# Optimization experiments

Measured on AMD Instinct MI355X. Metric: run time of the kernel, lower is better.

## Reference

```python
import jax, jax.numpy as jnp
import numpy as np

EPS = 1e-12  # tf.nn.l2_normalize epsilon used by keras Dot(normalize=True)

def _l2_normalize(x):
    # x: [..., D]; matches tf.nn.l2_normalize: x * rsqrt(max(sum(x^2), eps))
    sq = jnp.sum(x * x, axis=-1, keepdims=True)
    return x * jax.lax.rsqrt(jnp.maximum(sq, EPS))

def setup_inputs() -> dict:
    key = jax.random.key(0)
    k1, k2, k3 = jax.random.split(key, 3)
    B, L, D = 16, 1024, 1024
    a = jax.random.normal(k1, (B, L, D), dtype=jnp.float32)
    b = jax.random.normal(k2, (B, L, D), dtype=jnp.float32)
    # keras 'uniform' initializer: U(-0.05, 0.05)
    kernel = jax.random.uniform(k3, (D, 1), dtype=jnp.float32, minval=-0.05, maxval=0.05)
    return {"a": a, "b": b, "kernel": kernel}

def reference(a, b, kernel):
    # kernel: [D, 1] -> broadcastable weight vector [D]
    w = kernel[:, 0]
    # elementwise kernel weighting of both sequences: [B, L, D]
    ra = _l2_normalize(a * w)
    rb = _l2_normalize(b * w)
    # cosine-similarity matrix over sequence positions: [B, L, L]
    return jnp.einsum('bid,bjd->bij', ra, rb)
```

## Files before the change

### kernel.cpp

```cpp
#include <hip/hip_runtime.h>
#include <hip/hip_bf16.h>


typedef __bf16 bf16x8 __attribute__((ext_vector_type(8)));
typedef float f32x4 __attribute__((ext_vector_type(4)));

__device__ __forceinline__ unsigned short f2bf(float f) {
  __hip_bfloat16 h = __float2bfloat16(f);
  return *reinterpret_cast<unsigned short*>(&h);
}

__device__ __forceinline__ void gload16(const void* g, void* ldsp) {
  __builtin_amdgcn_global_load_lds(
      (const __attribute__((address_space(1))) unsigned int*)g,
      (__attribute__((address_space(3))) unsigned int*)ldsp,
      16, 0, 0);
}

__global__ void __launch_bounds__(256)
norm_scale_kernel(const float* __restrict__ a, const float* __restrict__ b,
                  const float* __restrict__ w, unsigned short* __restrict__ ra,
                  unsigned short* __restrict__ rb) {
  const int wave = threadIdx.x >> 6;
  const int lane = threadIdx.x & 63;
  const int row = blockIdx.x * 4 + wave;

  const float* src;
  unsigned short* dst;
  if (row < 16384) {
    src = a + (size_t)row * 1024;
    dst = ra + (size_t)row * 1024;
  } else {
    src = b + (size_t)(row - 16384) * 1024;
    dst = rb + (size_t)(row - 16384) * 1024;
  }

  float4 x[4];
  float sq = 0.f;
#pragma unroll
  for (int c = 0; c < 4; ++c) {
    float4 xv = *(const float4*)(src + c * 256 + lane * 4);
    float4 wv = *(const float4*)(w + c * 256 + lane * 4);
    xv.x *= wv.x; xv.y *= wv.y; xv.z *= wv.z; xv.w *= wv.w;
    x[c] = xv;
    sq += xv.x * xv.x + xv.y * xv.y + xv.z * xv.z + xv.w * xv.w;
  }
#pragma unroll
  for (int off = 32; off > 0; off >>= 1) sq += __shfl_xor(sq, off);
  const float s = rsqrtf(fmaxf(sq, 1e-12f));
#pragma unroll
  for (int c = 0; c < 4; ++c) {
    ushort4 u;
    u.x = f2bf(x[c].x * s);
    u.y = f2bf(x[c].y * s);
    u.z = f2bf(x[c].z * s);
    u.w = f2bf(x[c].w * s);
    *(ushort4*)(dst + c * 256 + lane * 4) = u;
  }
}

__global__ void __launch_bounds__(512, 2)
gemm8_kernel(const unsigned short* __restrict__ RA,
             const unsigned short* __restrict__ RB,
             float* __restrict__ C) {
  __shared__ __align__(16) char lds[131072];

  const int t = threadIdx.x;
  const int w = t >> 6, l = t & 63;
  const int wr = w >> 2, wc = w & 3;
  const int l4 = l & 15, lh = l >> 4;
  const int lr = l >> 3;
  const int lch = (l & 7) ^ lr;

  const int orig = (int)blockIdx.x;
  const int wgid = (orig & 7) * 32 + (orig >> 3);
  const int batch = wgid >> 4;
  const int tile = wgid & 15;
  const int brow_t = (tile >> 2) << 8;
  const int bcol_t = (tile & 3) << 8;

  const unsigned short* Ab = RA + ((size_t)batch << 20) + (size_t)brow_t * 1024;
  const unsigned short* Bb = RB + ((size_t)batch << 20) + (size_t)bcol_t * 1024;

  int aoff[2][2], boff[2][2];
#pragma unroll
  for (int h = 0; h < 2; ++h)
#pragma unroll
    for (int g = 0; g < 2; ++g) {
      const int rr = w * 16 + g * 8 + lr;
      const int ga = ((rr >> 6) << 7) + h * 64 + (rr & 63);
      const int gb = ((rr >> 5) << 6) + h * 32 + (rr & 31);
      aoff[h][g] = ga * 1024 + lch * 8;
      boff[h][g] = gb * 1024 + lch * 8;
    }
  const int stgw = w * 2048;

  const int arow = (wr * 64 + l4) * 128;
  const int brow = (wc * 32 + l4) * 128;
  int csw[2];
  csw[0] = ((0 + lh) ^ (l & 7)) * 16;
  csw[1] = ((4 + lh) ^ (l & 7)) * 16;

  f32x4 acc[8][4] = {};
  bf16x8 af[4][2], bq0[2][2], bq1[2][2];

#define STAGE_A(h, tau)                                                   \
  do {                                                                    \
    char* _d = lds + ((tau) & 1) * 65536 + (h) * 16384 + stgw;            \
    gload16(Ab + (size_t)aoff[h][0] + (size_t)(tau) * 64, _d);            \
    gload16(Ab + (size_t)aoff[h][1] + (size_t)(tau) * 64, _d + 1024);     \
  } while (0)
#define STAGE_B(h, tau)                                                   \
  do {                                                                    \
    char* _d = lds + ((tau) & 1) * 65536 + 32768 + (h) * 16384 + stgw;    \
    gload16(Bb + (size_t)boff[h][0] + (size_t)(tau) * 64, _d);            \
    gload16(Bb + (size_t)boff[h][1] + (size_t)(tau) * 64, _d + 1024);     \
  } while (0)
#define LDA(mh, bufbase)                                                  \
  _Pragma("unroll") for (int mm = 0; mm < 4; ++mm)                        \
  _Pragma("unroll") for (int ks = 0; ks < 2; ++ks)                        \
      af[mm][ks] = *(const bf16x8*)((bufbase) + (mh) * 16384 + arow +     \
                                    mm * 2048 + csw[ks]);
#define LDB(dst, nh, bufbase)                                             \
  _Pragma("unroll") for (int nn = 0; nn < 2; ++nn)                        \
  _Pragma("unroll") for (int ks = 0; ks < 2; ++ks)                        \
      dst[nn][ks] = *(const bf16x8*)((bufbase) + 32768 + (nh) * 16384 +   \
                                     brow + nn * 2048 + csw[ks]);
#define MQ(mh, nh, bsrc)                                                  \
  _Pragma("unroll") for (int mm = 0; mm < 4; ++mm)                        \
  _Pragma("unroll") for (int nn = 0; nn < 2; ++nn)                        \
  _Pragma("unroll") for (int ks = 0; ks < 2; ++ks)                        \
      acc[(mh) * 4 + mm][(nh) * 2 + nn] =                                 \
          __builtin_amdgcn_mfma_f32_16x16x32_bf16(                        \
              af[mm][ks], bsrc[nn][ks], acc[(mh) * 4 + mm][(nh) * 2 + nn],\
              0, 0, 0);
#define PHASE_PRE()                                                       \
  __builtin_amdgcn_s_barrier();                                           \
  asm volatile("s_waitcnt lgkmcnt(0)" ::: "memory");                      \
  __builtin_amdgcn_sched_barrier(0);                                      \
  __builtin_amdgcn_s_setprio(1)
#define PHASE_POST()                                                      \
  __builtin_amdgcn_s_setprio(0);                                          \
  __builtin_amdgcn_s_barrier()

  const char* b0 = lds;
  const char* b1 = lds + 65536;

  STAGE_A(0, 0); STAGE_B(0, 0); STAGE_B(1, 0); STAGE_A(1, 0);
  STAGE_A(0, 1); STAGE_B(0, 1); STAGE_B(1, 1);
  asm volatile("s_waitcnt vmcnt(6)" ::: "memory");
  __builtin_amdgcn_s_barrier();

#pragma unroll 1
  for (int i = 0; i < 7; ++i) {
    const int u = 2 * i;
    LDA(0, b0); LDB(bq0, 0, b0); STAGE_A(1, u + 1);
    PHASE_PRE(); MQ(0, 0, bq0); PHASE_POST();
    LDB(bq1, 1, b0); STAGE_A(0, u + 2);
    PHASE_PRE(); MQ(0, 1, bq1); PHASE_POST();
    LDA(1, b0); STAGE_B(0, u + 2);
    PHASE_PRE(); MQ(1, 1, bq1); PHASE_POST();
    STAGE_B(1, u + 2);
    asm volatile("s_waitcnt vmcnt(6)" ::: "memory");
    PHASE_PRE(); MQ(1, 0, bq0); PHASE_POST();
    LDA(0, b1); LDB(bq0, 0, b1); STAGE_A(1, u + 2);
    PHASE_PRE(); MQ(0, 0, bq0); PHASE_POST();
    LDB(bq1, 1, b1); STAGE_A(0, u + 3);
    PHASE_PRE(); MQ(0, 1, bq1); PHASE_POST();
    LDA(1, b1); STAGE_B(0, u + 3);
    PHASE_PRE(); MQ(1, 1, bq1); PHASE_POST();
    STAGE_B(1, u + 3);
    asm volatile("s_waitcnt vmcnt(6)" ::: "memory");
    PHASE_PRE(); MQ(1, 0, bq0); PHASE_POST();
  }

  LDA(0, b0); LDB(bq0, 0, b0); STAGE_A(1, 15);
  PHASE_PRE(); MQ(0, 0, bq0); PHASE_POST();
  LDB(bq1, 1, b0);
  PHASE_PRE(); MQ(0, 1, bq1); PHASE_POST();
  LDA(1, b0);
  PHASE_PRE(); MQ(1, 1, bq1); PHASE_POST();
  asm volatile("s_waitcnt vmcnt(0)" ::: "memory");
  PHASE_PRE(); MQ(1, 0, bq0); PHASE_POST();
  LDA(0, b1); LDB(bq0, 0, b1);
  PHASE_PRE(); MQ(0, 0, bq0); PHASE_POST();
  LDB(bq1, 1, b1);
  PHASE_PRE(); MQ(0, 1, bq1); PHASE_POST();
  LDA(1, b1);
  PHASE_PRE(); MQ(1, 1, bq1); PHASE_POST();
  PHASE_PRE(); MQ(1, 0, bq0); PHASE_POST();

#undef STAGE_A
#undef STAGE_B
#undef LDA
#undef LDB
#undef MQ
#undef PHASE_PRE
#undef PHASE_POST

  float* Cb = C + ((size_t)batch << 20);
  const int crow0 = brow_t + wr * 128 + lh * 4;
  const int ccol0 = bcol_t + wc * 64 + l4;
#pragma unroll
  for (int m = 0; m < 8; ++m)
#pragma unroll
    for (int n = 0; n < 4; ++n)
#pragma unroll
      for (int r = 0; r < 4; ++r)
        Cb[(size_t)(crow0 + m * 16 + r) * 1024 + ccol0 + n * 16] =
            acc[m][n][r];
}

extern "C" void kernel_launch(void* const* d_in, const int* in_sizes, int n_in,
                              void* d_out, int out_size, void* d_ws, size_t ws_size,
                              hipStream_t stream) {
  const float* a = (const float*)d_in[0];
  const float* b = (const float*)d_in[1];
  const float* w = (const float*)d_in[2];
  float* out = (float*)d_out;

  unsigned short* ra = (unsigned short*)d_ws;
  unsigned short* rb = ra + (size_t)16 * 1024 * 1024;

  norm_scale_kernel<<<8192, 256, 0, stream>>>(a, b, w, ra, rb);
  gemm8_kernel<<<256, 512, 0, stream>>>(ra, rb, out);
}
```

Before: 204.0 us.

## Fuse weighting and L2 normalization into GEMM with epilogue norm scaling

Removes the separate normalize-and-convert kernel; the GEMM now loads fp32 inputs, applies the weight, converts to bf16 into LDS, and accumulates per-row squared norms, applying rsqrt scales to the output in the epilogue. This avoids the intermediate bf16 workspace round trip and a second launch. In exchange, each block re-reads fp32 rows redundantly across tiles and replaces the async global-to-LDS pipeline with register-staged loads and simpler barrier scheduling, which may expose memory latency.

```diff
diff --git a/kernel.cpp b/kernel.cpp
--- a/kernel.cpp
+++ b/kernel.cpp
@@ -4,66 +4,19 @@
 
 typedef __bf16 bf16x8 __attribute__((ext_vector_type(8)));
 typedef float f32x4 __attribute__((ext_vector_type(4)));
+typedef unsigned short us8 __attribute__((ext_vector_type(8)));
 
 __device__ __forceinline__ unsigned short f2bf(float f) {
   __hip_bfloat16 h = __float2bfloat16(f);
   return *reinterpret_cast<unsigned short*>(&h);
 }
 
-__device__ __forceinline__ void gload16(const void* g, void* ldsp) {
-  __builtin_amdgcn_global_load_lds(
-      (const __attribute__((address_space(1))) unsigned int*)g,
-      (__attribute__((address_space(3))) unsigned int*)ldsp,
-      16, 0, 0);
-}
-
-__global__ void __launch_bounds__(256)
-norm_scale_kernel(const float* __restrict__ a, const float* __restrict__ b,
-                  const float* __restrict__ w, unsigned short* __restrict__ ra,
-                  unsigned short* __restrict__ rb) {
-  const int wave = threadIdx.x >> 6;
-  const int lane = threadIdx.x & 63;
-  const int row = blockIdx.x * 4 + wave;
-
-  const float* src;
-  unsigned short* dst;
-  if (row < 16384) {
-    src = a + (size_t)row * 1024;
-    dst = ra + (size_t)row * 1024;
-  } else {
-    src = b + (size_t)(row - 16384) * 1024;
-    dst = rb + (size_t)(row - 16384) * 1024;
-  }
-
-  float4 x[4];
-  float sq = 0.f;
-#pragma unroll
-  for (int c = 0; c < 4; ++c) {
-    float4 xv = *(const float4*)(src + c * 256 + lane * 4);
-    float4 wv = *(const float4*)(w + c * 256 + lane * 4);
-    xv.x *= wv.x; xv.y *= wv.y; xv.z *= wv.z; xv.w *= wv.w;
-    x[c] = xv;
-    sq += xv.x * xv.x + xv.y * xv.y + xv.z * xv.z + xv.w * xv.w;
-  }
-#pragma unroll
-  for (int off = 32; off > 0; off >>= 1) sq += __shfl_xor(sq, off);
-  const float s = rsqrtf(fmaxf(sq, 1e-12f));
-#pragma unroll
-  for (int c = 0; c < 4; ++c) {
-    ushort4 u;
-    u.x = f2bf(x[c].x * s);
-    u.y = f2bf(x[c].y * s);
-    u.z = f2bf(x[c].z * s);
-    u.w = f2bf(x[c].w * s);
-    *(ushort4*)(dst + c * 256 + lane * 4) = u;
-  }
-}
-
 __global__ void __launch_bounds__(512, 2)
-gemm8_kernel(const unsigned short* __restrict__ RA,
-             const unsigned short* __restrict__ RB,
-             float* __restrict__ C) {
+fused_kernel(const float* __restrict__ A, const float* __restrict__ Bm,
+             const float* __restrict__ W, float* __restrict__ C) {
   __shared__ __align__(16) char lds[131072];
+  __shared__ __align__(16) float wlds[1024];
+  __shared__ float nAl[256], nBl[256];
 
   const int t = threadIdx.x;
   const int w = t >> 6, l = t & 63;
@@ -79,10 +32,10 @@
   const int brow_t = (tile >> 2) << 8;
   const int bcol_t = (tile & 3) << 8;
 
-  const unsigned short* Ab = RA + ((size_t)batch << 20) + (size_t)brow_t * 1024;
-  const unsigned short* Bb = RB + ((size_t)batch << 20) + (size_t)bcol_t * 1024;
-
-  int aoff[2][2], boff[2][2];
+  const float* Af = A + ((size_t)batch << 20) + (size_t)brow_t * 1024;
+  const float* Bf = Bm + ((size_t)batch << 20) + (size_t)bcol_t * 1024;
+
+  int aoffs[2][2], boffs[2][2], garow[2][2], gbrow[2][2];
 #pragma unroll
   for (int h = 0; h < 2; ++h)
 #pragma unroll
@@ -90,8 +43,9 @@
       const int rr = w * 16 + g * 8 + lr;
       const int ga = ((rr >> 6) << 7) + h * 64 + (rr & 63);
       const int gb = ((rr >> 5) << 6) + h * 32 + (rr & 31);
-      aoff[h][g] = ga * 1024 + lch * 8;
-      boff[h][g] = gb * 1024 + lch * 8;
+      garow[h][g] = ga; gbrow[h][g] = gb;
+      aoffs[h][g] = ga * 1024 + lch * 8;
+      boffs[h][g] = gb * 1024 + lch * 8;
     }
   const int stgw = w * 2048;
 
@@ -102,113 +56,150 @@
   csw[1] = ((4 + lh) ^ (l & 7)) * 16;
 
   f32x4 acc[8][4] = {};
-  bf16x8 af[4][2], bq0[2][2], bq1[2][2];
-
-#define STAGE_A(h, tau)                                                   \
-  do {                                                                    \
-    char* _d = lds + ((tau) & 1) * 65536 + (h) * 16384 + stgw;            \
-    gload16(Ab + (size_t)aoff[h][0] + (size_t)(tau) * 64, _d);            \
-    gload16(Ab + (size_t)aoff[h][1] + (size_t)(tau) * 64, _d + 1024);     \
-  } while (0)
-#define STAGE_B(h, tau)                                                   \
-  do {                                                                    \
-    char* _d = lds + ((tau) & 1) * 65536 + 32768 + (h) * 16384 + stgw;    \
-    gload16(Bb + (size_t)boff[h][0] + (size_t)(tau) * 64, _d);            \
-    gload16(Bb + (size_t)boff[h][1] + (size_t)(tau) * 64, _d + 1024);     \
-  } while (0)
-#define LDA(mh, bufbase)                                                  \
+  bf16x8 af[4][2], bq[2][2];
+  float nsq[8] = {0.f, 0.f, 0.f, 0.f, 0.f, 0.f, 0.f, 0.f};
+  float4 xv[2][2];
+  float4 ws0, ws1;
+
+  if (t < 256) ((float4*)wlds)[t] = ((const float4*)W)[t];
+  __syncthreads();
+
+#define ALOAD(h, t1)                                                      \
+  _Pragma("unroll") for (int g = 0; g < 2; ++g) {                         \
+    const float* _p = Af + aoffs[h][g] + (t1) * 64;                       \
+    xv[g][0] = *(const float4*)_p;                                        \
+    xv[g][1] = *(const float4*)(_p + 4);                                  \
+  }
+#define BLOAD(h, t1)                                                      \
+  _Pragma("unroll") for (int g = 0; g < 2; ++g) {                         \
+    const float* _p = Bf + boffs[h][g] + (t1) * 64;                       \
+    xv[g][0] = *(const float4*)_p;                                        \
+    xv[g][1] = *(const float4*)(_p + 4);                                  \
+  }
+#define WSLICE(t1)                                                        \
+  ws0 = *(const float4*)(wlds + (t1) * 64 + lch * 8);                     \
+  ws1 = *(const float4*)(wlds + (t1) * 64 + lch * 8 + 4);
+#define CVTW(isB, h, nxtbase)                                             \
+  _Pragma("unroll") for (int g = 0; g < 2; ++g) {                         \
+    float4 v0, v1;                                                        \
+    v0.x = xv[g][0].x * ws0.x; v0.y = xv[g][0].y * ws0.y;                 \
+    v0.z = xv[g][0].z * ws0.z; v0.w = xv[g][0].w * ws0.w;                 \
+    v1.x = xv[g][1].x * ws1.x; v1.y = xv[g][1].y * ws1.y;                 \
+    v1.z = xv[g][1].z * ws1.z; v1.w = xv[g][1].w * ws1.w;                 \
+    nsq[(isB) * 4 + (h) * 2 + g] +=                                       \
+        v0.x * v0.x + v0.y * v0.y + v0.z * v0.z + v0.w * v0.w +           \
+        v1.x * v1.x + v1.y * v1.y + v1.z * v1.z + v1.w * v1.w;            \
+    us8 pk;                                                               \
+    pk[0] = f2bf(v0.x); pk[1] = f2bf(v0.y);                               \
+    pk[2] = f2bf(v0.z); pk[3] = f2bf(v0.w);                               \
+    pk[4] = f2bf(v1.x); pk[5] = f2bf(v1.y);                               \
+    pk[6] = f2bf(v1.z); pk[7] = f2bf(v1.w);                               \
+    *(us8*)((nxtbase) + (isB) * 32768 + (h) * 16384 + stgw + g * 1024 +   \
+            l * 16) = pk;                                                 \
+  }
+#define LDAF(mh, bufb)                                                    \
   _Pragma("unroll") for (int mm = 0; mm < 4; ++mm)                        \
   _Pragma("unroll") for (int ks = 0; ks < 2; ++ks)                        \
-      af[mm][ks] = *(const bf16x8*)((bufbase) + (mh) * 16384 + arow +     \
+      af[mm][ks] = *(const bf16x8*)((bufb) + (mh) * 16384 + arow +        \
                                     mm * 2048 + csw[ks]);
-#define LDB(dst, nh, bufbase)                                             \
+#define LDBQ(nh, bufb)                                                    \
   _Pragma("unroll") for (int nn = 0; nn < 2; ++nn)                        \
   _Pragma("unroll") for (int ks = 0; ks < 2; ++ks)                        \
-      dst[nn][ks] = *(const bf16x8*)((bufbase) + 32768 + (nh) * 16384 +   \
-                                     brow + nn * 2048 + csw[ks]);
-#define MQ(mh, nh, bsrc)                                                  \
+      bq[nn][ks] = *(const bf16x8*)((bufb) + 32768 + (nh) * 16384 +       \
+                                    brow + nn * 2048 + csw[ks]);
+#define MQ(mh, nh)                                                        \
+  __builtin_amdgcn_s_setprio(1);                                          \
   _Pragma("unroll") for (int mm = 0; mm < 4; ++mm)                        \
   _Pragma("unroll") for (int nn = 0; nn < 2; ++nn)                        \
   _Pragma("unroll") for (int ks = 0; ks < 2; ++ks)                        \
       acc[(mh) * 4 + mm][(nh) * 2 + nn] =                                 \
           __builtin_amdgcn_mfma_f32_16x16x32_bf16(                        \
-              af[mm][ks], bsrc[nn][ks], acc[(mh) * 4 + mm][(nh) * 2 + nn],\
-              0, 0, 0);
-#define PHASE_PRE()                                                       \
-  __builtin_amdgcn_s_barrier();                                           \
-  asm volatile("s_waitcnt lgkmcnt(0)" ::: "memory");                      \
-  __builtin_amdgcn_sched_barrier(0);                                      \
-  __builtin_amdgcn_s_setprio(1)
-#define PHASE_POST()                                                      \
-  __builtin_amdgcn_s_setprio(0);                                          \
-  __builtin_amdgcn_s_barrier()
-
-  const char* b0 = lds;
-  const char* b1 = lds + 65536;
-
-  STAGE_A(0, 0); STAGE_B(0, 0); STAGE_B(1, 0); STAGE_A(1, 0);
-  STAGE_A(0, 1); STAGE_B(0, 1); STAGE_B(1, 1);
-  asm volatile("s_waitcnt vmcnt(6)" ::: "memory");
-  __builtin_amdgcn_s_barrier();
+              af[mm][ks], bq[nn][ks], acc[(mh) * 4 + mm][(nh) * 2 + nn],  \
+              0, 0, 0);                                                   \
+  __builtin_amdgcn_s_setprio(0);
+
+  char* b0p = lds;
+  char* b1p = lds + 65536;
+
+  WSLICE(0);
+  ALOAD(0, 0); CVTW(0, 0, b0p);
+  ALOAD(1, 0); CVTW(0, 1, b0p);
+  BLOAD(0, 0); CVTW(1, 0, b0p);
+  BLOAD(1, 0); CVTW(1, 1, b0p);
+  __syncthreads();
 
 #pragma unroll 1
-  for (int i = 0; i < 7; ++i) {
-    const int u = 2 * i;
-    LDA(0, b0); LDB(bq0, 0, b0); STAGE_A(1, u + 1);
-    PHASE_PRE(); MQ(0, 0, bq0); PHASE_POST();
-    LDB(bq1, 1, b0); STAGE_A(0, u + 2);
-    PHASE_PRE(); MQ(0, 1, bq1); PHASE_POST();
-    LDA(1, b0); STAGE_B(0, u + 2);
-    PHASE_PRE(); MQ(1, 1, bq1); PHASE_POST();
-    STAGE_B(1, u + 2);
-    asm volatile("s_waitcnt vmcnt(6)" ::: "memory");
-    PHASE_PRE(); MQ(1, 0, bq0); PHASE_POST();
-    LDA(0, b1); LDB(bq0, 0, b1); STAGE_A(1, u + 2);
-    PHASE_PRE(); MQ(0, 0, bq0); PHASE_POST();
-    LDB(bq1, 1, b1); STAGE_A(0, u + 3);
-    PHASE_PRE(); MQ(0, 1, bq1); PHASE_POST();
-    LDA(1, b1); STAGE_B(0, u + 3);
-    PHASE_PRE(); MQ(1, 1, bq1); PHASE_POST();
-    STAGE_B(1, u + 3);
-    asm volatile("s_waitcnt vmcnt(6)" ::: "memory");
-    PHASE_PRE(); MQ(1, 0, bq0); PHASE_POST();
-  }
-
-  LDA(0, b0); LDB(bq0, 0, b0); STAGE_A(1, 15);
-  PHASE_PRE(); MQ(0, 0, bq0); PHASE_POST();
-  LDB(bq1, 1, b0);
-  PHASE_PRE(); MQ(0, 1, bq1); PHASE_POST();
-  LDA(1, b0);
-  PHASE_PRE(); MQ(1, 1, bq1); PHASE_POST();
-  asm volatile("s_waitcnt vmcnt(0)" ::: "memory");
-  PHASE_PRE(); MQ(1, 0, bq0); PHASE_POST();
-  LDA(0, b1); LDB(bq0, 0, b1);
-  PHASE_PRE(); MQ(0, 0, bq0); PHASE_POST();
-  LDB(bq1, 1, b1);
-  PHASE_PRE(); MQ(0, 1, bq1); PHASE_POST();
-  LDA(1, b1);
-  PHASE_PRE(); MQ(1, 1, bq1); PHASE_POST();
-  PHASE_PRE(); MQ(1, 0, bq0); PHASE_POST();
-
-#undef STAGE_A
-#undef STAGE_B
-#undef LDA
-#undef LDB
+  for (int kt = 0; kt < 15; ++kt) {
+    char* cur = (kt & 1) ? b1p : b0p;
+    char* nxt = (kt & 1) ? b0p : b1p;
+    WSLICE(kt + 1);
+    ALOAD(0, kt + 1);
+    LDBQ(0, cur); LDAF(0, cur);
+    MQ(0, 0);
+    CVTW(0, 0, nxt);
+    ALOAD(1, kt + 1);
+    LDBQ(1, cur);
+    MQ(0, 1);
+    CVTW(0, 1, nxt);
+    BLOAD(0, kt + 1);
+    LDAF(1, cur); LDBQ(0, cur);
+    MQ(1, 0);
+    CVTW(1, 0, nxt);
+    BLOAD(1, kt + 1);
+    LDBQ(1, cur);
+    MQ(1, 1);
+    CVTW(1, 1, nxt);
+    __syncthreads();
+  }
+  {
+    char* cur = b1p;
+    LDBQ(0, cur); LDAF(0, cur); MQ(0, 0);
+    LDBQ(1, cur); MQ(0, 1);
+    LDAF(1, cur); LDBQ(0, cur); MQ(1, 0);
+    LDBQ(1, cur); MQ(1, 1);
+  }
+
+#undef ALOAD
+#undef BLOAD
+#undef WSLICE
+#undef CVTW
+#undef LDAF
+#undef LDBQ
 #undef MQ
-#undef PHASE_PRE
-#undef PHASE_POST
+
+#pragma unroll
+  for (int i = 0; i < 8; ++i) {
+    nsq[i] += __shfl_xor(nsq[i], 1);
+    nsq[i] += __shfl_xor(nsq[i], 2);
+    nsq[i] += __shfl_xor(nsq[i], 4);
+  }
+  if ((l & 7) == 0) {
+#pragma unroll
+    for (int h = 0; h < 2; ++h)
+#pragma unroll
+      for (int g = 0; g < 2; ++g) {
+        nAl[garow[h][g]] = rsqrtf(fmaxf(nsq[h * 2 + g], 1e-12f));
+        nBl[gbrow[h][g]] = rsqrtf(fmaxf(nsq[4 + h * 2 + g], 1e-12f));
+      }
+  }
+  __syncthreads();
 
   float* Cb = C + ((size_t)batch << 20);
   const int crow0 = brow_t + wr * 128 + lh * 4;
   const int ccol0 = bcol_t + wc * 64 + l4;
+  float fbv[4];
+#pragma unroll
+  for (int n = 0; n < 4; ++n) fbv[n] = nBl[wc * 64 + l4 + n * 16];
 #pragma unroll
   for (int m = 0; m < 8; ++m)
 #pragma unroll
-    for (int n = 0; n < 4; ++n)
-#pragma unroll
-      for (int r = 0; r < 4; ++r)
+    for (int r = 0; r < 4; ++r) {
+      const float fav = nAl[wr * 128 + lh * 4 + m * 16 + r];
+#pragma unroll
+      for (int n = 0; n < 4; ++n)
         Cb[(size_t)(crow0 + m * 16 + r) * 1024 + ccol0 + n * 16] =
-            acc[m][n][r];
+            acc[m][n][r] * fav * fbv[n];
+    }
 }
 
 extern "C" void kernel_launch(void* const* d_in, const int* in_sizes, int n_in,
@@ -219,9 +210,5 @@
   const float* w = (const float*)d_in[2];
   float* out = (float*)d_out;
 
-  unsigned short* ra = (unsigned short*)d_ws;
-  unsigned short* rb = ra + (size_t)16 * 1024 * 1024;
-
-  norm_scale_kernel<<<8192, 256, 0, stream>>>(a, b, w, ra, rb);
-  gemm8_kernel<<<256, 512, 0, stream>>>(ra, rb, out);
+  fused_kernel<<<256, 512, 0, stream>>>(a, b, w, out);
 }
```

Measured after the change: 199.4 us. 2.2% less time.
